# Performance work log

Measured on AMD Instinct MI355X. Metric: run time of the kernel, lower is better.

## Reference

```python
import jax, jax.numpy as jnp
import numpy as np

N = 64      # features
L = 96      # history length
LP = 24     # prediction length
H = 128     # rnn hidden
B = 1024    # batch


def setup_inputs() -> dict:
    key = jax.random.key(0)
    ks = jax.random.split(key, 16)
    # monotonically increasing timestamps
    tp_all = jnp.cumsum(jax.random.uniform(ks[0], (B, L + LP), dtype=jnp.float32), axis=1)
    tp_true = tp_all[:, :L]
    tp_pred = tp_all[:, L:]
    X = jax.random.normal(ks[1], (B, L, N), dtype=jnp.float32)
    mask = jax.random.randint(ks[2], (B, L, N), 0, 2).astype(jnp.float32)
    def unif(k, shape, fan):
        std = 1.0 / np.sqrt(fan)
        return jax.random.uniform(k, shape, jnp.float32, -std, std)
    # TemporalDecay for h: W (H,N), b (H); std = 1/sqrt(out)
    Wh_dec = unif(ks[3], (H, N), H)
    bh_dec = unif(ks[4], (H,), H)
    # TemporalDecay for x (diag): W (N,N) but only diagonal used
    Wx_dec = unif(ks[5], (N, N), N)
    bx_dec = unif(ks[6], (N,), N)
    # GRUCell: input size = 2N + H
    in_sz = 2 * N + H
    W_ih = unif(ks[7], (3 * H, in_sz), H)
    W_hh = unif(ks[8], (3 * H, H), H)
    b_ih = unif(ks[9], (3 * H,), H)
    b_hh = unif(ks[10], (3 * H,), H)
    # output projection
    Wp = unif(ks[11], (N, H), H)
    bp = unif(ks[12], (N,), H)
    return {"tp_pred": tp_pred, "X": X, "tp_true": tp_true, "mask": mask,
            "Wh_dec": Wh_dec, "bh_dec": bh_dec, "Wx_dec": Wx_dec, "bx_dec": bx_dec,
            "W_ih": W_ih, "W_hh": W_hh, "b_ih": b_ih, "b_hh": b_hh,
            "Wp": Wp, "bp": bp}


def _grud(tp_pred, X, tp_true, mask, Wh_dec, bh_dec, Wx_dec, bx_dec,
          W_ih, W_hh, b_ih, b_hh, Wp, bp):
    Bsz, Lh, Nf = X.shape
    Lp = tp_pred.shape[1]
    Lall = Lh + Lp
    Hh = Wh_dec.shape[0]

    # pad future with zeros (unobserved)
    X_all = jnp.concatenate([X, jnp.zeros((Bsz, Lp, Nf), X.dtype)], axis=1)
    M_all = jnp.concatenate([mask, jnp.zeros((Bsz, Lp, Nf), X.dtype)], axis=1)
    tp = jnp.concatenate([tp_true, tp_pred], axis=1)

    # deltas: first-difference padded with 0 at t=0, broadcast over features
    dt = jnp.pad(tp[:, 1:] - tp[:, :-1], ((0, 0), (1, 0)))  # (B, Lall)
    deltas = jnp.broadcast_to(dt[:, :, None], (Bsz, Lall, Nf))

    # empirical mean over positions where (1 - mask) == 1 (faithful to source)
    valid = 1.0 - M_all
    cnt = jnp.clip(valid.sum(axis=1), 1.0, None)  # (B, N)
    mu = (X_all * valid).sum(axis=1) / cnt        # (B, N)

    # LOCF as in source: where mask != 0, copy previous value
    def locf_step(prev, xm):
        x_t, m_t = xm
        cur = jnp.where(m_t != 0, prev, x_t)
        return cur, cur
    _, X_locf = jax.lax.scan(locf_step, X_all[:, 0],
                             (jnp.swapaxes(X_all, 0, 1), jnp.swapaxes(M_all, 0, 1)))
    # X_locf: (Lall, B, N)

    diag_Wx = jnp.diag(Wx_dec)  # (N,) -- diag=True masks W with identity

    def step(h, inputs):
        x_t, m_t, d_t, xl_t = inputs  # each (B, N)
        gh = jnp.exp(-jax.nn.relu(d_t @ Wh_dec.T + bh_dec))      # (B, H)
        gx = jnp.exp(-jax.nn.relu(d_t * diag_Wx + bx_dec))       # (B, N)
        h = h * gh
        rep = h
        x_h = gx * xl_t + (1.0 - gx) * mu
        x_in = m_t * x_t + (1.0 - m_t) * x_h
        inp = jnp.concatenate([x_in, h, m_t], axis=1)             # (B, 2N+H)
        gi = inp @ W_ih.T + b_ih                                  # (B, 3H)
        gr = h @ W_hh.T + b_hh                                    # (B, 3H)
        r = jax.nn.sigmoid(gi[:, :Hh] + gr[:, :Hh])
        z = jax.nn.sigmoid(gi[:, Hh:2 * Hh] + gr[:, Hh:2 * Hh])
        n = jnp.tanh(gi[:, 2 * Hh:] + r * gr[:, 2 * Hh:])
        h_new = (1.0 - z) * n + z * h
        return h_new, rep

    h0 = jnp.zeros((Bsz, Hh), X.dtype)
    xs = (jnp.swapaxes(X_all, 0, 1), jnp.swapaxes(M_all, 0, 1),
          jnp.swapaxes(deltas, 0, 1), X_locf)
    _, reps = jax.lax.scan(step, h0, xs)          # (Lall, B, H)
    reps = jnp.swapaxes(reps, 0, 1)               # (B, Lall, H)
    recon = reps @ Wp.T + bp                      # (B, Lall, N)
    y_hat = recon[:, -Lp:]                        # (B, Lp, N)
    return y_hat[None]                            # (1, B, Lp, N)


def reference(tp_pred, X, tp_true, mask, Wh_dec, bh_dec, Wx_dec, bx_dec,
              W_ih, W_hh, b_ih, b_hh, Wp, bp):
    return _grud(tp_pred, X, tp_true, mask, Wh_dec, bh_dec, Wx_dec, bx_dec,
                 W_ih, W_hh, b_ih, b_hh, Wp, bp)
```

## Files before the change

kernel.cpp:

```cpp
#include <hip/hip_runtime.h>

#define L2E 1.4426950408889634f

typedef _Float16 f16x8 __attribute__((ext_vector_type(8)));
typedef _Float16 f16x4 __attribute__((ext_vector_type(4)));
typedef float f32x4 __attribute__((ext_vector_type(4)));

__device__ __forceinline__ float sig_fast(float x) {
    return __builtin_amdgcn_rcpf(1.0f + __builtin_amdgcn_exp2f(-L2E * x));
}
__device__ __forceinline__ float tanh_fast(float x) {
    return 1.0f - 2.0f * __builtin_amdgcn_rcpf(1.0f + __builtin_amdgcn_exp2f(2.0f * L2E * x));
}
__device__ __forceinline__ float expnr_fast(float x) {
    return __builtin_amdgcn_exp2f(-L2E * fmaxf(x, 0.0f));
}
__device__ __forceinline__ void barrier_lds_only() {
    __asm__ volatile("s_waitcnt lgkmcnt(0)\n\ts_barrier" ::: "memory");
}

struct F8 { float v[8]; };
__device__ __forceinline__ F8 ld8(const float* p) {
    F8 r;
    float4 a = *(const float4*)p, b = *(const float4*)(p + 4);
    r.v[0]=a.x; r.v[1]=a.y; r.v[2]=a.z; r.v[3]=a.w;
    r.v[4]=b.x; r.v[5]=b.y; r.v[6]=b.z; r.v[7]=b.w;
    return r;
}
__device__ __forceinline__ f16x8 cvt8(F8 a) {
    f16x8 r;
#pragma unroll
    for (int q = 0; q < 8; ++q) r[q] = (_Float16)a.v[q];
    return r;
}
__device__ __forceinline__ f16x8 cvt8s(F8 a, F8 b) {
    f16x8 r;
#pragma unroll
    for (int q = 0; q < 8; ++q) r[q] = (_Float16)(a.v[q] + b.v[q]);
    return r;
}

__global__ __launch_bounds__(768, 3) void grud_kernel(
    const float* __restrict__ tp_pred, const float* __restrict__ X,
    const float* __restrict__ tp_true, const float* __restrict__ mask,
    const float* __restrict__ Wh_dec, const float* __restrict__ bh_dec,
    const float* __restrict__ Wx_dec, const float* __restrict__ bx_dec,
    const float* __restrict__ W_ih, const float* __restrict__ W_hh,
    const float* __restrict__ b_ih, const float* __restrict__ b_hh,
    const float* __restrict__ Wp, const float* __restrict__ bp,
    float* __restrict__ out)
{
    constexpr int SR = 136;
    __shared__ alignas(16) _Float16 ring[8 * 2048];
    __shared__ alignas(16) _Float16 V[2][16 * SR];
    __shared__ alignas(16) _Float16 Astage[16 * SR];
    __shared__ float dt_lds[480];
    __shared__ float mu_l[4][64];
    __shared__ float wxl[64], bxl[64];

    const int tid  = threadIdx.x;
    const int w    = tid >> 6, l = tid & 63, quad = l >> 4, lm = l & 15;
    const int b0   = blockIdx.x * 4;

    for (int i = tid; i < 16 * SR; i += 768) ((unsigned*)V)[i] = 0;

    if (tid < 480) {
        int t = tid >> 2, q = tid & 3, b = b0 + q;
        float v = 0.0f;
        if (t) {
            float cur = (t < 96) ? tp_true[b * 96 + t] : tp_pred[b * 24 + t - 96];
            float prv = (t - 1 < 96) ? tp_true[b * 96 + t - 1] : tp_pred[b * 24 + t - 97];
            v = cur - prv;
        }
        dt_lds[tid] = v;
    }
    if (tid < 64) { wxl[tid] = Wx_dec[tid * 65]; bxl[tid] = bx_dec[tid]; }

    if (w >= 8) {
        const int pw   = w - 8;
        const int ptid = tid - 512;
        const int c0   = 32 * pw + lm, c1 = c0 + 16;

        {
            const float* xr = X    + ((size_t)(b0 + pw) * 96) * 64 + l;
            const float* mr = mask + ((size_t)(b0 + pw) * 96) * 64 + l;
            float a = 0.0f, c = 0.0f;
#pragma unroll 4
            for (int t = 0; t < 96; ++t) {
                float x = xr[t * 64], m = mr[t * 64];
                a += x * (1.0f - m); c += 1.0f - m;
            }
            mu_l[pw][l] = a / (c + 24.0f);
        }

        f16x8 wxf[3][2][4];
#pragma unroll
        for (int g = 0; g < 3; ++g)
#pragma unroll
            for (int j = 0; j < 2; ++j)
#pragma unroll
                for (int fi = 0; fi < 4; ++fi) {
                    const int row = g * 128 + (j ? c1 : c0);
                    const int k0 = fi * 32 + quad * 8;
                    wxf[g][j][fi] = cvt8(ld8(W_ih + row * 256 + (k0 < 64 ? k0 : 128 + k0)));
                }

        const int pn = pw * 16 + lm;
        const float bpv = bp[pn];
        f16x8 wPf[4];
#pragma unroll
        for (int fi = 0; fi < 4; ++fi)
            wPf[fi] = cvt8(ld8(Wp + pn * 128 + fi * 32 + quad * 8));

        auto prodLoad = [&](int gp, float4& px, float4& pm) {
            if (gp >= 24) { px = make_float4(0,0,0,0); pm = make_float4(0,0,0,0); return; }
            const int R = ptid >> 4, tg = 4 * gp + (R >> 2), b = R & 3;
            const size_t o = (((size_t)(b0 + b) * 96) + tg) * 64 + (ptid & 15) * 4;
            px = *(const float4*)(X + o);
            pm = *(const float4*)(mask + o);
        };
        auto prodStage = [&](int gp, float4 px, float4 pm) {
            const int R = ptid >> 4, toff = R >> 2, b = R & 3;
            const int tg = 4 * gp + toff, n0 = (ptid & 15) * 4;
            const float d = dt_lds[tg * 4 + b];
            const float xs[4] = {px.x, px.y, px.z, px.w};
            const float ms[4] = {pm.x, pm.y, pm.z, pm.w};
            f16x4 xi, mm;
#pragma unroll
            for (int e = 0; e < 4; ++e) {
                const int n = n0 + e;
                const float gxv = expnr_fast(d * wxl[n] + bxl[n]);
                const float muv = mu_l[b][n];
                float v;
                if (gp < 24) {
                    v = (ms[e] != 0.0f) ? xs[e] : (xs[e] - muv) * gxv + muv;
                    mm[e] = (_Float16)ms[e];
                } else {
                    v = (1.0f - gxv) * muv;
                    mm[e] = (_Float16)0.0f;
                }
                xi[e] = (_Float16)v;
            }
            *(f16x4*)&Astage[R * SR + n0]      = xi;
            *(f16x4*)&Astage[R * SR + 64 + n0] = mm;
        };
        auto prodMMA = [&](int gp, int j) {
            f16x8 ap[4];
#pragma unroll
            for (int fi = 0; fi < 4; ++fi)
                ap[fi] = *(const f16x8*)&Astage[lm * SR + fi * 32 + quad * 8];
            const int c = j ? c1 : c0;
            const int slot = (4 * gp + quad) & 7;
            f32x4 aR = {0,0,0,0}, aZ = {0,0,0,0}, aN = {0,0,0,0};
#pragma unroll
            for (int fi = 0; fi < 4; ++fi) {
                aR = __builtin_amdgcn_mfma_f32_16x16x32_f16(ap[fi], wxf[0][j][fi], aR, 0, 0, 0);
                aZ = __builtin_amdgcn_mfma_f32_16x16x32_f16(ap[fi], wxf[1][j][fi], aZ, 0, 0, 0);
                aN = __builtin_amdgcn_mfma_f32_16x16x32_f16(ap[fi], wxf[2][j][fi], aN, 0, 0, 0);
            }
#pragma unroll
            for (int rb = 0; rb < 4; ++rb) {
                f16x4 pk = {(_Float16)aR[rb], (_Float16)aZ[rb], (_Float16)aN[rb], (_Float16)0.0f};
                *(f16x4*)&ring[slot * 2048 + c * 16 + rb * 4] = pk;
            }
        };

        __syncthreads();
        {
            float4 px, pm;
            prodLoad(0, px, pm);
            prodStage(0, px, pm);
            barrier_lds_only();
            prodMMA(0, 0); prodMMA(0, 1);
            barrier_lds_only();
        }

        float4 px, pm;
        for (int t = 0; t < 120; ++t) {
            const int gp = (t >> 2) + 1, ph = t & 3;
            if (ph == 0)      { if (gp < 30) prodLoad(gp, px, pm); }
            else if (ph == 1) { if (gp < 30) prodStage(gp, px, pm); }
            else if (ph == 2) { if (gp < 30) prodMMA(gp, 0); }
            else              { if (gp < 30) prodMMA(gp, 1); }

            if (t >= 96) {
                f16x8 af[4];
#pragma unroll
                for (int fi = 0; fi < 4; ++fi)
                    af[fi] = *(const f16x8*)&V[t & 1][lm * SR + fi * 32 + quad * 8];
                f32x4 aP = {bpv, 0, 0, 0};
#pragma unroll
                for (int fi = 0; fi < 4; ++fi)
                    aP = __builtin_amdgcn_mfma_f32_16x16x32_f16(af[fi], wPf[fi], aP, 0, 0, 0);
                out[((size_t)(b0 + quad) * 24 + (t - 96)) * 64 + pn] = aP[0];
            }
            barrier_lds_only();
        }
    } else {
        const int c = 16 * w + lm;

        f16x8 wR[4], wZ[4], wN[4], wG[4];
#pragma unroll
        for (int fi = 0; fi < 4; ++fi) {
            const int k0 = fi * 32 + quad * 8;
            wR[fi] = cvt8s(ld8(W_ih + c * 256 + 64 + k0),
                           ld8(W_hh + c * 128 + k0));
            wZ[fi] = cvt8s(ld8(W_ih + (128 + c) * 256 + 64 + k0),
                           ld8(W_hh + (128 + c) * 128 + k0));
            wN[fi] = cvt8(ld8(W_ih + (256 + c) * 256 + 64 + k0));
            wG[fi] = cvt8(ld8(W_hh + (256 + c) * 128 + k0));
        }
        float S = 0.0f;
        {
            const float4* wh4 = (const float4*)(Wh_dec + c * 64);
#pragma unroll
            for (int i = 0; i < 16; ++i) { float4 u = wh4[i]; S += u.x + u.y + u.z + u.w; }
        }
        const float bhc = bh_dec[c];
        const float bRc = b_ih[c] + b_hh[c];
        const float bZc = b_ih[128 + c] + b_hh[128 + c];
        const float bNc = b_ih[256 + c];
        const float bGc = b_hh[256 + c];

        __syncthreads();
        barrier_lds_only();
        barrier_lds_only();

        const f32x4 ZV = {0.0f, 0.0f, 0.0f, 0.0f};
        float h = 0.0f;
        for (int t = 0; t < 120; ++t) {
            const _Float16* Vp = V[t & 1];
            const f16x4 g = *(const f16x4*)&ring[(t & 7) * 2048 + c * 16 + quad * 4];
            f16x8 af[4];
#pragma unroll
            for (int fi = 0; fi < 4; ++fi)
                af[fi] = *(const f16x8*)&Vp[lm * SR + fi * 32 + quad * 8];

            const int tn = (t < 119) ? t + 1 : 119;
            const float ghd = expnr_fast(dt_lds[tn * 4 + quad] * S + bhc);

            f32x4 aR = __builtin_amdgcn_mfma_f32_16x16x32_f16(af[0], wR[0], ZV, 0, 0, 0);
            f32x4 aZ = __builtin_amdgcn_mfma_f32_16x16x32_f16(af[0], wZ[0], ZV, 0, 0, 0);
            f32x4 aN = __builtin_amdgcn_mfma_f32_16x16x32_f16(af[0], wN[0], ZV, 0, 0, 0);
            f32x4 aG = __builtin_amdgcn_mfma_f32_16x16x32_f16(af[0], wG[0], ZV, 0, 0, 0);
#pragma unroll
            for (int fi = 1; fi < 4; ++fi) {
                aR = __builtin_amdgcn_mfma_f32_16x16x32_f16(af[fi], wR[fi], aR, 0, 0, 0);
                aZ = __builtin_amdgcn_mfma_f32_16x16x32_f16(af[fi], wZ[fi], aZ, 0, 0, 0);
                aN = __builtin_amdgcn_mfma_f32_16x16x32_f16(af[fi], wN[fi], aN, 0, 0, 0);
                aG = __builtin_amdgcn_mfma_f32_16x16x32_f16(af[fi], wG[fi], aG, 0, 0, 0);
            }

            const float rg = sig_fast(aR[0] + ((float)g[0] + bRc));
            const float zg = sig_fast(aZ[0] + ((float)g[1] + bZc));
            const float ng = tanh_fast(aN[0] + ((float)g[2] + bNc) + rg * (aG[0] + bGc));
            h = (zg * (h - ng) + ng) * ghd;
            if (t < 119)
                V[(t & 1) ^ 1][(4 * quad) * SR + c] = (_Float16)h;
            barrier_lds_only();
        }
    }
}

extern "C" void kernel_launch(void* const* d_in, const int* in_sizes, int n_in,
                              void* d_out, int out_size, void* d_ws, size_t ws_size,
                              hipStream_t stream) {
    const float* tp_pred = (const float*)d_in[0];
    const float* X       = (const float*)d_in[1];
    const float* tp_true = (const float*)d_in[2];
    const float* mask    = (const float*)d_in[3];
    const float* Wh_dec  = (const float*)d_in[4];
    const float* bh_dec  = (const float*)d_in[5];
    const float* Wx_dec  = (const float*)d_in[6];
    const float* bx_dec  = (const float*)d_in[7];
    const float* W_ih    = (const float*)d_in[8];
    const float* W_hh    = (const float*)d_in[9];
    const float* b_ih    = (const float*)d_in[10];
    const float* b_hh    = (const float*)d_in[11];
    const float* Wp      = (const float*)d_in[12];
    const float* bp      = (const float*)d_in[13];

    grud_kernel<<<dim3(256), dim3(768), 0, stream>>>(
        tp_pred, X, tp_true, mask, Wh_dec, bh_dec, Wx_dec, bx_dec,
        W_ih, W_hh, b_ih, b_hh, Wp, bp, (float*)d_out);
}
```

Before: 209.8 us.

## Halve batch rows per block and double grid to spread recurrence across more CUs

Each block now handles 2 batch rows instead of 4, and the grid grows from 256 to 512 blocks so more CUs run the serial recurrence at once. The gate-input ring buffer, dt table and mu table shrink to match, and the ring is re-indexed so only the valid MFMA rows are written. Launch bounds ask for 6 blocks per CU to keep occupancy up. The trade is that half of each 16-row MFMA tile is now padding, so per-block compute efficiency drops, and the 96-register-per-thread cap at 6 blocks per CU risks spilling the many weight fragments held in registers.

```diff
diff --git a/kernel.cpp b/kernel.cpp
--- a/kernel.cpp
+++ b/kernel.cpp
@@ -40,7 +40,7 @@
     return r;
 }
 
-__global__ __launch_bounds__(768, 3) void grud_kernel(
+__global__ __launch_bounds__(768, 6) void grud_kernel(
     const float* __restrict__ tp_pred, const float* __restrict__ X,
     const float* __restrict__ tp_true, const float* __restrict__ mask,
     const float* __restrict__ Wh_dec, const float* __restrict__ bh_dec,
@@ -51,21 +51,23 @@
     float* __restrict__ out)
 {
     constexpr int SR = 136;
-    __shared__ alignas(16) _Float16 ring[8 * 2048];
+    constexpr int RS = 1032;
+    __shared__ alignas(16) _Float16 ring[8 * RS];
     __shared__ alignas(16) _Float16 V[2][16 * SR];
     __shared__ alignas(16) _Float16 Astage[16 * SR];
-    __shared__ float dt_lds[480];
-    __shared__ float mu_l[4][64];
+    __shared__ float dt_lds[240];
+    __shared__ float mu_l[2][64];
     __shared__ float wxl[64], bxl[64];
 
     const int tid  = threadIdx.x;
     const int w    = tid >> 6, l = tid & 63, quad = l >> 4, lm = l & 15;
-    const int b0   = blockIdx.x * 4;
+    const int b0   = blockIdx.x * 2;
 
     for (int i = tid; i < 16 * SR; i += 768) ((unsigned*)V)[i] = 0;
-
-    if (tid < 480) {
-        int t = tid >> 2, q = tid & 3, b = b0 + q;
+    for (int i = tid; i < 8 * SR; i += 768) ((unsigned*)Astage)[i] = 0;
+
+    if (tid < 240) {
+        int t = tid >> 1, b = b0 + (tid & 1);
         float v = 0.0f;
         if (t) {
             float cur = (t < 96) ? tp_true[b * 96 + t] : tp_pred[b * 24 + t - 96];
@@ -81,7 +83,7 @@
         const int ptid = tid - 512;
         const int c0   = 32 * pw + lm, c1 = c0 + 16;
 
-        {
+        if (pw < 2) {
             const float* xr = X    + ((size_t)(b0 + pw) * 96) * 64 + l;
             const float* mr = mask + ((size_t)(b0 + pw) * 96) * 64 + l;
             float a = 0.0f, c = 0.0f;
@@ -113,16 +115,20 @@
             wPf[fi] = cvt8(ld8(Wp + pn * 128 + fi * 32 + quad * 8));
 
         auto prodLoad = [&](int gp, float4& px, float4& pm) {
-            if (gp >= 24) { px = make_float4(0,0,0,0); pm = make_float4(0,0,0,0); return; }
-            const int R = ptid >> 4, tg = 4 * gp + (R >> 2), b = R & 3;
+            px = make_float4(0,0,0,0); pm = make_float4(0,0,0,0);
+            const int R = ptid >> 4;
+            if (gp >= 24 || R >= 8) return;
+            const int tg = 4 * gp + (R >> 1), b = R & 1;
             const size_t o = (((size_t)(b0 + b) * 96) + tg) * 64 + (ptid & 15) * 4;
             px = *(const float4*)(X + o);
             pm = *(const float4*)(mask + o);
         };
         auto prodStage = [&](int gp, float4 px, float4 pm) {
-            const int R = ptid >> 4, toff = R >> 2, b = R & 3;
+            const int R = ptid >> 4;
+            if (R >= 8) return;
+            const int toff = R >> 1, b = R & 1;
             const int tg = 4 * gp + toff, n0 = (ptid & 15) * 4;
-            const float d = dt_lds[tg * 4 + b];
+            const float d = dt_lds[tg * 2 + b];
             const float xs[4] = {px.x, px.y, px.z, px.w};
             const float ms[4] = {pm.x, pm.y, pm.z, pm.w};
             f16x4 xi, mm;
@@ -150,7 +156,6 @@
             for (int fi = 0; fi < 4; ++fi)
                 ap[fi] = *(const f16x8*)&Astage[lm * SR + fi * 32 + quad * 8];
             const int c = j ? c1 : c0;
-            const int slot = (4 * gp + quad) & 7;
             f32x4 aR = {0,0,0,0}, aZ = {0,0,0,0}, aN = {0,0,0,0};
 #pragma unroll
             for (int fi = 0; fi < 4; ++fi) {
@@ -158,10 +163,14 @@
                 aZ = __builtin_amdgcn_mfma_f32_16x16x32_f16(ap[fi], wxf[1][j][fi], aZ, 0, 0, 0);
                 aN = __builtin_amdgcn_mfma_f32_16x16x32_f16(ap[fi], wxf[2][j][fi], aN, 0, 0, 0);
             }
-#pragma unroll
-            for (int rb = 0; rb < 4; ++rb) {
-                f16x4 pk = {(_Float16)aR[rb], (_Float16)aZ[rb], (_Float16)aN[rb], (_Float16)0.0f};
-                *(f16x4*)&ring[slot * 2048 + c * 16 + rb * 4] = pk;
+            if (quad < 2) {
+#pragma unroll
+                for (int rb = 0; rb < 4; ++rb) {
+                    const int slot = (4 * gp + 2 * quad + (rb >> 1)) & 7;
+                    const int b = rb & 1;
+                    f16x4 pk = {(_Float16)aR[rb], (_Float16)aZ[rb], (_Float16)aN[rb], (_Float16)0.0f};
+                    *(f16x4*)&ring[slot * RS + ((b << 7) + c) * 4] = pk;
+                }
             }
         };
 
@@ -192,7 +201,8 @@
 #pragma unroll
                 for (int fi = 0; fi < 4; ++fi)
                     aP = __builtin_amdgcn_mfma_f32_16x16x32_f16(af[fi], wPf[fi], aP, 0, 0, 0);
-                out[((size_t)(b0 + quad) * 24 + (t - 96)) * 64 + pn] = aP[0];
+                if (quad < 2)
+                    out[((size_t)(b0 + quad) * 24 + (t - 96)) * 64 + pn] = aP[0];
             }
             barrier_lds_only();
         }
@@ -227,17 +237,18 @@
         barrier_lds_only();
 
         const f32x4 ZV = {0.0f, 0.0f, 0.0f, 0.0f};
+        const int bq = quad & 1;
         float h = 0.0f;
         for (int t = 0; t < 120; ++t) {
             const _Float16* Vp = V[t & 1];
-            const f16x4 g = *(const f16x4*)&ring[(t & 7) * 2048 + c * 16 + quad * 4];
+            const f16x4 g = *(const f16x4*)&ring[(t & 7) * RS + ((bq << 7) + c) * 4];
             f16x8 af[4];
 #pragma unroll
             for (int fi = 0; fi < 4; ++fi)
                 af[fi] = *(const f16x8*)&Vp[lm * SR + fi * 32 + quad * 8];
 
             const int tn = (t < 119) ? t + 1 : 119;
-            const float ghd = expnr_fast(dt_lds[tn * 4 + quad] * S + bhc);
+            const float ghd = expnr_fast(dt_lds[tn * 2 + bq] * S + bhc);
 
             f32x4 aR = __builtin_amdgcn_mfma_f32_16x16x32_f16(af[0], wR[0], ZV, 0, 0, 0);
             f32x4 aZ = __builtin_amdgcn_mfma_f32_16x16x32_f16(af[0], wZ[0], ZV, 0, 0, 0);
@@ -255,7 +266,7 @@
             const float zg = sig_fast(aZ[0] + ((float)g[1] + bZc));
             const float ng = tanh_fast(aN[0] + ((float)g[2] + bNc) + rg * (aG[0] + bGc));
             h = (zg * (h - ng) + ng) * ghd;
-            if (t < 119)
+            if (t < 119 && quad < 2)
                 V[(t & 1) ^ 1][(4 * quad) * SR + c] = (_Float16)h;
             barrier_lds_only();
         }
@@ -280,7 +291,7 @@
     const float* Wp      = (const float*)d_in[12];
     const float* bp      = (const float*)d_in[13];
 
-    grud_kernel<<<dim3(256), dim3(768), 0, stream>>>(
+    grud_kernel<<<dim3(512), dim3(768), 0, stream>>>(
         tp_pred, X, tp_true, mask, Wh_dec, bh_dec, Wx_dec, bx_dec,
         W_ih, W_hh, b_ih, b_hh, Wp, bp, (float*)d_out);
 }
```

Result: slower. 681.5 us (+224.9%).
